# Kernel optimization log

Hardware: AMD Instinct MI355X
Metric: run time of the kernel (lower is better)

Reference implementation:

```python
import jax, jax.numpy as jnp
import numpy as np

D, K, CIN, CD, COUT = 3, 16, 128, 32, 256
C = CIN + CD                  # 160 = C_in + C_delta after concat
DM = -(-COUT // C)            # depth_multiplier = ceil(C_out / C) = 2
N, I = 4, 2048                # batch, points per cloud; M = N*I = 8192


def _bn(x, g, b, eps=1e-5):
    # BatchNorm1d in training mode: biased batch statistics over dim 0
    mu = x.mean(0)
    v = x.var(0)
    return (x - mu) * jax.lax.rsqrt(v + eps) * g + b


def _knn(p, k):
    # knn_graph over ALL M points (wrapper passes no batch vector), loop=True
    d2 = jnp.sum(p * p, axis=1)
    dist = d2[:, None] + d2[None, :] - 2.0 * (p @ p.T)   # [M,M]
    _, idx = jax.lax.top_k(-dist, k)                     # [M,K], self first
    return idx


def _gconv(t, w, b, M):
    # grouped Conv1d(K, K*K, kernel=K, groups=K): t [M,K,K], w [K(cin), K(out/grp), K(tap)]
    return jnp.einsum('mcl,col->mco', t, w).reshape(M, K * K) + b


def _xconv(xf, pf, idx, w1a, b1a, g1a, be1a, w1b, b1b, g1b, be1b,
           w2, b2, g2a, be2a, wc2a, bc2a, g2b, be2b, wc2b, bc2b, g2c, be2c,
           wcd, bcd, wl, bl):
    M = pf.shape[0]
    rel = pf[idx] - pf[:, None, :]                       # [M,K,D] relative neighbor coords
    # mlp1: lift relative coords to C_delta features
    h = rel.reshape(M * K, D)
    h = _bn(jax.nn.elu(h @ w1a + b1a), g1a, be1a)
    h = _bn(jax.nn.elu(h @ w1b + b1b), g1b, be1b)
    x_star = jnp.concatenate([h.reshape(M, K, CD), xf[idx]], axis=-1)  # [M,K,C]
    x_star = x_star.transpose(0, 2, 1)                   # [M,C,K]
    # mlp2: learn KxK X-transformation from the K*D relative coords
    t = _bn(jax.nn.elu(rel.reshape(M, K * D) @ w2 + b2), g2a, be2a).reshape(M, K, K)
    t = _bn(jax.nn.elu(_gconv(t, wc2a, bc2a, M)), g2b, be2b).reshape(M, K, K)
    t = _bn(_gconv(t, wc2b, bc2b, M), g2c, be2c).reshape(M, K, K)
    xt = jnp.einsum('mck,mkj->mcj', x_star, t)           # [M,C,K] batched matmul
    # depthwise Conv1d(C, C*DM, K, groups=C) collapses K, then final Linear
    y = jnp.einsum('mcl,col->mco', xt, wcd).reshape(M, C * DM) + bcd
    return y @ wl + bl                                   # [M,COUT]


def setup_inputs() -> dict:
    key = jax.random.key(0)
    ks = jax.random.split(key, 16)
    r = lambda k, s: jax.random.normal(k, s, jnp.float32) * 0.1
    return dict(
        x=jax.random.normal(ks[0], (N, I, CIN), jnp.float32),
        pos=jax.random.normal(ks[1], (N, I, D), jnp.float32),
        w1a=r(ks[2], (D, CD)), b1a=r(ks[3], (CD,)), g1a=jnp.ones((CD,)), be1a=jnp.zeros((CD,)),
        w1b=r(ks[4], (CD, CD)), b1b=r(ks[5], (CD,)), g1b=jnp.ones((CD,)), be1b=jnp.zeros((CD,)),
        w2=r(ks[6], (D * K, K * K)), b2=r(ks[7], (K * K,)), g2a=jnp.ones((K * K,)), be2a=jnp.zeros((K * K,)),
        wc2a=r(ks[8], (K, K, K)), bc2a=r(ks[9], (K * K,)), g2b=jnp.ones((K * K,)), be2b=jnp.zeros((K * K,)),
        wc2b=r(ks[10], (K, K, K)), bc2b=r(ks[11], (K * K,)), g2c=jnp.ones((K * K,)), be2c=jnp.zeros((K * K,)),
        wcd=r(ks[12], (C, DM, K)), bcd=r(ks[13], (C * DM,)),
        wl=r(ks[14], (C * DM, COUT)), bl=r(ks[15], (COUT,)),
    )


def reference(x, pos, w1a, b1a, g1a, be1a, w1b, b1b, g1b, be1b,
              w2, b2, g2a, be2a, wc2a, bc2a, g2b, be2b, wc2b, bc2b, g2c, be2c,
              wcd, bcd, wl, bl):
    pf = pos.reshape(N * I, D)
    xf = x.reshape(N * I, CIN)
    idx = _knn(pf, K)
    out = _xconv(xf, pf, idx, w1a, b1a, g1a, be1a, w1b, b1b, g1b, be1b,
                 w2, b2, g2a, be2a, wc2a, bc2a, g2b, be2b, wc2b, bc2b, g2c, be2c,
                 wcd, bcd, wl, bl)
    return out.reshape(N, I, COUT)
```

## Files before the change

kernel.cpp:

```cpp
#include <hip/hip_runtime.h>
#include <math.h>

#define M_PTS 8192
#define MK    131072

__device__ __forceinline__ float elu(float v){ return v > 0.f ? v : __expf(v)-1.0f; }

__device__ __forceinline__ unsigned distkey(float4 c, float qx, float qy, float qz, float d2q){
  #pragma clang fp contract(off)
  float dot  = __builtin_fmaf(c.z, qz, __builtin_fmaf(c.y, qy, __builtin_fmaf(c.x, qx, 0.0f)));
  float A    = d2q + c.w;
  float B    = 2.0f * dot;
  float dist = A - B;
  unsigned u = __float_as_uint(dist);
  return u ^ ((unsigned)((int)u >> 31) | 0x80000000u);
}

__global__ __launch_bounds__(256) void knn_kernel(const float* __restrict__ pos,
                                                  int* __restrict__ nidx,
                                                  float* __restrict__ st){
  #pragma clang fp contract(off)
  __shared__ float4 cand[1024];
  __shared__ unsigned long long hits[4][64];
  int tid  = threadIdx.x;
  int lane = tid & 63;
  int wv   = tid >> 6;
  int q    = blockIdx.x*4 + wv;
  if (blockIdx.x == 0){
    for (int i = tid; i < 2048; i += 256) st[i] = 0.f;
  }
  float qx = pos[3*q], qy = pos[3*q+1], qz = pos[3*q+2];
  float d2q = (qx*qx + qy*qy) + qz*qz;

  unsigned ka[8];
  #pragma unroll
  for (int s=0;s<8;s++) ka[s] = 0xFFFFFFFFu;

  for (int base = 0; base < M_PTS; base += 1024){
    for (int t = tid; t < 1024; t += 256){
      int j = base + t;
      float x = pos[3*j], y = pos[3*j+1], z = pos[3*j+2];
      float d2v = (x*x + y*y) + z*z;
      cand[t] = make_float4(x,y,z,d2v);
    }
    __syncthreads();
    #pragma unroll
    for (int k=0; k<16; k++){
      unsigned v = distkey(cand[lane + k*64], qx, qy, qz, d2q);
      #pragma unroll
      for (int s=0;s<8;s++){
        unsigned mn = min(v, ka[s]);
        unsigned mx = max(v, ka[s]);
        ka[s] = mn; v = mx;
      }
    }
    __syncthreads();
  }

  unsigned thr = 0xFFFFFFFFu;
  for (int r=0; r<16; r++){
    unsigned mine = ka[0];
    unsigned best = mine;
    #pragma unroll
    for (int off=32; off>0; off>>=1){
      unsigned o = __shfl_xor(best, off, 64);
      best = min(best, o);
    }
    bool adv = (best == mine);
    #pragma unroll
    for (int s=0;s<7;s++) ka[s] = adv ? ka[s+1] : ka[s];
    ka[7] = adv ? 0xFFFFFFFFu : ka[7];
    thr = best;
  }

  int cnt = 0;
  for (int base = 0; base < M_PTS; base += 1024){
    for (int t = tid; t < 1024; t += 256){
      int j = base + t;
      float x = pos[3*j], y = pos[3*j+1], z = pos[3*j+2];
      float d2v = (x*x + y*y) + z*z;
      cand[t] = make_float4(x,y,z,d2v);
    }
    __syncthreads();
    #pragma unroll
    for (int k=0; k<16; k++){
      int j = base + lane + k*64;
      unsigned u = distkey(cand[lane + k*64], qx, qy, qz, d2q);
      bool hit = (u <= thr);
      unsigned long long m = __ballot(hit);
      if (hit){
        int slot = cnt + __popcll(m & ((1ull<<lane)-1ull));
        if (slot < 64) hits[wv][slot] = ((unsigned long long)u << 32) | (unsigned)j;
      }
      cnt += (int)__popcll(m);
    }
    __syncthreads();
  }

  int cc = min(cnt, 64);
  unsigned long long mine = (lane < cc) ? hits[wv][lane] : ~0ull;
  for (int r=0; r<16; r++){
    unsigned long long best = mine;
    #pragma unroll
    for (int off=32; off>0; off>>=1){
      unsigned long long o = __shfl_xor(best, off, 64);
      best = (o < best) ? o : best;
    }
    if (mine == best) mine = ~0ull;
    if (lane == 0) nidx[q*16 + r] = (int)(unsigned)best;
  }
}

#define COMPUTE_RELF_8(OFFS)                                          \
  for (int f = tid; f < 8*48; f += 256){                              \
    int p = f/48, kd = f%48, k = kd/3, d = kd%3;                      \
    int j = nidx[(m0+p)*16 + k];                                      \
    relf[p][kd] = pos[3*j+d] - pos[3*(m0+p)+d];                       \
  }                                                                   \
  __syncthreads();

#define COMPUTE_T1_8(acc)                                             \
  _Pragma("unroll")                                                   \
  for (int p=0;p<8;p++) acc[p] = b2[tid];                             \
  for (int kk=0; kk<48; kk++){                                        \
    float w = w2[kk*256 + tid];                                       \
    _Pragma("unroll")                                                 \
    for (int p=0;p<8;p++) acc[p] += relf[p][kk]*w;                    \
  }

__global__ __launch_bounds__(256) void stats_a_kernel(const float* __restrict__ pos,
    const int* __restrict__ nidx,
    const float* __restrict__ w1a, const float* __restrict__ b1a,
    const float* __restrict__ w2,  const float* __restrict__ b2,
    float* __restrict__ s1, float* __restrict__ s3){
  int tid = threadIdx.x;
  if (blockIdx.x < 512){
    __shared__ float relS[256][3];
    __shared__ float red[8][64];
    int r = blockIdx.x*256 + tid;
    int m = r >> 4;
    int j = nidx[r];
    relS[tid][0] = pos[3*j  ]-pos[3*m  ];
    relS[tid][1] = pos[3*j+1]-pos[3*m+1];
    relS[tid][2] = pos[3*j+2]-pos[3*m+2];
    __syncthreads();
    int c = tid & 31, g = tid >> 5;
    float w0=w1a[c], w1v=w1a[32+c], w2v=w1a[64+c], b=b1a[c];
    float s=0.f, q=0.f;
    for (int rr=g*32; rr<g*32+32; rr++){
      float h = elu(b + relS[rr][0]*w0 + relS[rr][1]*w1v + relS[rr][2]*w2v);
      s += h; q += h*h;
    }
    red[g][c]=s; red[g][32+c]=q;
    __syncthreads();
    if (tid < 64){
      float a=0.f;
      #pragma unroll
      for (int gg=0;gg<8;gg++) a += red[gg][tid];
      atomicAdd(&s1[tid], a);
    }
  } else {
    __shared__ float relf[8][48];
    int m0 = (blockIdx.x-512)*8;
    COMPUTE_RELF_8();
    float acc[8];
    COMPUTE_T1_8(acc);
    float s=0.f, q=0.f;
    #pragma unroll
    for (int p=0;p<8;p++){ float v = elu(acc[p]); s += v; q += v*v; }
    atomicAdd(&s3[tid], s); atomicAdd(&s3[256+tid], q);
  }
}

__global__ __launch_bounds__(256) void stats_b_kernel(const float* __restrict__ pos,
    const int* __restrict__ nidx,
    const float* __restrict__ w1a, const float* __restrict__ b1a,
    const float* __restrict__ s1,  const float* __restrict__ g1a, const float* __restrict__ be1a,
    const float* __restrict__ w1b, const float* __restrict__ b1b,
    const float* __restrict__ w2,  const float* __restrict__ b2,
    const float* __restrict__ s3,  const float* __restrict__ g2a, const float* __restrict__ be2a,
    const float* __restrict__ wc2a,const float* __restrict__ bc2a,
    float* __restrict__ s2, float* __restrict__ s4){
  int tid = threadIdx.x;
  const float invMK = 1.f/(float)MK;
  const float invM  = 1.f/8192.f;
  if (blockIdx.x < 2048){
    __shared__ float xnS[64][33];
    __shared__ float red[8][64];
    __shared__ float muA[32], ivA[32];
    if (tid < 32){
      float mu  = s1[tid]*invMK;
      float var = s1[32+tid]*invMK - mu*mu;
      muA[tid] = mu; ivA[tid] = rsqrtf(var+1e-5f)*g1a[tid];
    }
    __syncthreads();
    {
      int rl = tid >> 2;
      int r  = blockIdx.x*64 + rl;
      int m = r >> 4;
      int j = nidx[r];
      float rx = pos[3*j]-pos[3*m], ry = pos[3*j+1]-pos[3*m+1], rz = pos[3*j+2]-pos[3*m+2];
      int c0 = (tid & 3)*8;
      #pragma unroll
      for (int u=0; u<8; u++){
        int cc = c0 + u;
        float h = elu(b1a[cc] + rx*w1a[cc] + ry*w1a[32+cc] + rz*w1a[64+cc]);
        xnS[rl][cc] = (h-muA[cc])*ivA[cc] + be1a[cc];
      }
    }
    __syncthreads();
    int o = tid & 31, g = tid >> 5;
    float wcol[32];
    #pragma unroll
    for (int cc=0;cc<32;cc++) wcol[cc] = w1b[cc*32+o];
    float bo = b1b[o], s=0.f, q=0.f;
    for (int rr=g*8; rr<g*8+8; rr++){
      float a = bo;
      #pragma unroll
      for (int cc=0;cc<32;cc++) a += xnS[rr][cc]*wcol[cc];
      float v = elu(a);
      s += v; q += v*v;
    }
    red[g][o]=s; red[g][32+o]=q;
    __syncthreads();
    if (tid < 64){
      float a=0.f;
      #pragma unroll
      for (int gg=0;gg<8;gg++) a += red[gg][tid];
      atomicAdd(&s2[tid], a);
    }
  } else {
    __shared__ float relf[8][48];
    __shared__ float tn[8][256];
    int m0 = (blockIdx.x-2048)*8;
    COMPUTE_RELF_8();
    float acc[8];
    COMPUTE_T1_8(acc);
    float mu3  = s3[tid]*invM;
    float var3 = s3[256+tid]*invM - mu3*mu3;
    float i3   = rsqrtf(var3+1e-5f)*g2a[tid];
    float bb3  = be2a[tid];
    #pragma unroll
    for (int p=0;p<8;p++) tn[p][tid] = (elu(acc[p])-mu3)*i3 + bb3;
    __syncthreads();
    int c = tid >> 4;
    float wreg[16];
    const float4* wv4 = (const float4*)(wc2a + tid*16);
    #pragma unroll
    for (int v=0; v<4; v++){ float4 f = wv4[v]; wreg[4*v]=f.x; wreg[4*v+1]=f.y; wreg[4*v+2]=f.z; wreg[4*v+3]=f.w; }
    float bias = bc2a[tid];
    float s=0.f, q=0.f;
    #pragma unroll
    for (int p=0;p<8;p++){
      float a2 = bias;
      #pragma unroll
      for (int l=0;l<16;l++) a2 += tn[p][c*16+l]*wreg[l];
      float v = elu(a2);
      s += v; q += v*v;
    }
    atomicAdd(&s4[tid], s); atomicAdd(&s4[256+tid], q);
  }
}

__global__ __launch_bounds__(256) void t3_stats_kernel(const float* __restrict__ pos,
    const int* __restrict__ nidx, const float* __restrict__ w2, const float* __restrict__ b2,
    const float* __restrict__ s3, const float* __restrict__ g2a, const float* __restrict__ be2a,
    const float* __restrict__ wc2a, const float* __restrict__ bc2a,
    const float* __restrict__ s4, const float* __restrict__ g2b, const float* __restrict__ be2b,
    const float* __restrict__ wc2b, const float* __restrict__ bc2b, float* __restrict__ s5){
  __shared__ float relf[8][48];
  __shared__ float tn[8][256];
  __shared__ float tn2[8][256];
  int m0 = blockIdx.x*8, tid = threadIdx.x;
  const float invM = 1.f/8192.f;
  COMPUTE_RELF_8();
  float acc[8];
  COMPUTE_T1_8(acc);
  float mu3  = s3[tid]*invM;
  float var3 = s3[256+tid]*invM - mu3*mu3;
  float i3   = rsqrtf(var3+1e-5f)*g2a[tid];
  float bb3  = be2a[tid];
  #pragma unroll
  for (int p=0;p<8;p++) tn[p][tid] = (elu(acc[p])-mu3)*i3 + bb3;
  __syncthreads();
  int c = tid >> 4;
  float wreg[16];
  { const float4* wv4 = (const float4*)(wc2a + tid*16);
    #pragma unroll
    for (int v=0; v<4; v++){ float4 f = wv4[v]; wreg[4*v]=f.x; wreg[4*v+1]=f.y; wreg[4*v+2]=f.z; wreg[4*v+3]=f.w; } }
  float bias = bc2a[tid];
  float mu4  = s4[tid]*invM;
  float var4 = s4[256+tid]*invM - mu4*mu4;
  float i4   = rsqrtf(var4+1e-5f)*g2b[tid];
  float bb4  = be2b[tid];
  float t2v[8];
  #pragma unroll
  for (int p=0;p<8;p++){
    float a2 = bias;
    #pragma unroll
    for (int l=0;l<16;l++) a2 += tn[p][c*16+l]*wreg[l];
    t2v[p] = elu(a2);
  }
  #pragma unroll
  for (int p=0;p<8;p++) tn2[p][tid] = (t2v[p]-mu4)*i4 + bb4;
  __syncthreads();
  float w2reg[16];
  { const float4* wv4 = (const float4*)(wc2b + tid*16);
    #pragma unroll
    for (int v=0; v<4; v++){ float4 f = wv4[v]; w2reg[4*v]=f.x; w2reg[4*v+1]=f.y; w2reg[4*v+2]=f.z; w2reg[4*v+3]=f.w; } }
  float bias2 = bc2b[tid];
  float s=0.f, q=0.f;
  #pragma unroll
  for (int p=0;p<8;p++){
    float a3 = bias2;
    #pragma unroll
    for (int l=0;l<16;l++) a3 += tn2[p][c*16+l]*w2reg[l];
    s += a3; q += a3*a3;
  }
  atomicAdd(&s5[tid], s); atomicAdd(&s5[256+tid], q);
}

#define PF 4
__global__ __launch_bounds__(256) void final_kernel(
    const float* __restrict__ x, const float* __restrict__ pos, const int* __restrict__ nidx,
    const float* __restrict__ w1a, const float* __restrict__ b1a,
    const float* __restrict__ g1a, const float* __restrict__ be1a,
    const float* __restrict__ w1b, const float* __restrict__ b1b,
    const float* __restrict__ g1b, const float* __restrict__ be1b,
    const float* __restrict__ w2,  const float* __restrict__ b2,
    const float* __restrict__ g2a, const float* __restrict__ be2a,
    const float* __restrict__ wc2a,const float* __restrict__ bc2a,
    const float* __restrict__ g2b, const float* __restrict__ be2b,
    const float* __restrict__ wc2b,const float* __restrict__ bc2b,
    const float* __restrict__ g2c, const float* __restrict__ be2c,
    const float* __restrict__ wcd, const float* __restrict__ bcd,
    const float* __restrict__ wl,  const float* __restrict__ bl,
    const float* __restrict__ st,
    float* __restrict__ out){
  __shared__ float relf[PF][48];
  __shared__ float tA[PF][256];
  __shared__ float tB[PF][256];
  __shared__ float xs[PF*32*17];
  __shared__ float yy[PF][320];
  __shared__ int   sidx[PF*16];
  __shared__ float mu1[32], i1g[32], mu2[32], i2g[32];
  int tid = threadIdx.x;
  int m0  = blockIdx.x*PF;
  const float invMK = 1.f/(float)MK;
  const float invM  = 1.f/8192.f;

  if (tid < PF*16) sidx[tid] = nidx[m0*16 + tid];
  for (int f = tid; f < PF*48; f += 256){
    int p = f/48, kd = f%48, k = kd/3, d = kd%3;
    int j = nidx[(m0+p)*16 + k];
    relf[p][kd] = pos[3*j+d] - pos[3*(m0+p)+d];
  }
  if (tid < 32){
    float mu  = st[tid]*invMK;
    float var = st[32+tid]*invMK - mu*mu;
    mu1[tid] = mu; i1g[tid] = rsqrtf(var+1e-5f)*g1a[tid];
    float mu_2  = st[64+tid]*invMK;
    float var_2 = st[96+tid]*invMK - mu_2*mu_2;
    mu2[tid] = mu_2; i2g[tid] = rsqrtf(var_2+1e-5f)*g1b[tid];
  }
  float mu3 = st[128+tid]*invM, var3 = st[384+tid]*invM - mu3*mu3;
  float i3 = rsqrtf(var3+1e-5f)*g2a[tid], bb3 = be2a[tid];
  float mu4 = st[640+tid]*invM, var4 = st[896+tid]*invM - mu4*mu4;
  float i4 = rsqrtf(var4+1e-5f)*g2b[tid], bb4 = be2b[tid];
  float mu5 = st[1152+tid]*invM, var5 = st[1408+tid]*invM - mu5*mu5;
  float i5 = rsqrtf(var5+1e-5f)*g2c[tid], bb5 = be2c[tid];
  __syncthreads();

  {
    float a[PF];
    #pragma unroll
    for (int p=0;p<PF;p++) a[p] = b2[tid];
    for (int kk=0; kk<48; kk++){
      float w = w2[kk*256 + tid];
      #pragma unroll
      for (int p=0;p<PF;p++) a[p] += relf[p][kk]*w;
    }
    #pragma unroll
    for (int p=0;p<PF;p++) tA[p][tid] = (elu(a[p])-mu3)*i3 + bb3;
  }
  __syncthreads();

  int c = tid >> 4;
  {
    float wreg[16];
    const float4* wv4 = (const float4*)(wc2a + tid*16);
    #pragma unroll
    for (int v=0; v<4; v++){ float4 f = wv4[v]; wreg[4*v]=f.x; wreg[4*v+1]=f.y; wreg[4*v+2]=f.z; wreg[4*v+3]=f.w; }
    float bias = bc2a[tid];
    float t2v[PF];
    #pragma unroll
    for (int p=0;p<PF;p++){
      float a2 = bias;
      #pragma unroll
      for (int l=0;l<16;l++) a2 += tA[p][c*16+l]*wreg[l];
      t2v[p] = elu(a2);
    }
    #pragma unroll
    for (int p=0;p<PF;p++) tB[p][tid] = (t2v[p]-mu4)*i4 + bb4;
  }
  __syncthreads();

  {
    float w2reg[16];
    const float4* wv4 = (const float4*)(wc2b + tid*16);
    #pragma unroll
    for (int v=0; v<4; v++){ float4 f = wv4[v]; w2reg[4*v]=f.x; w2reg[4*v+1]=f.y; w2reg[4*v+2]=f.z; w2reg[4*v+3]=f.w; }
    float bias2 = bc2b[tid];
    #pragma unroll
    for (int p=0;p<PF;p++){
      float a3 = bias2;
      #pragma unroll
      for (int l=0;l<16;l++) a3 += tB[p][c*16+l]*w2reg[l];
      tA[p][tid] = (a3-mu5)*i5 + bb5;
    }
  }

  {
    int row = tid >> 2;
    int p = row >> 4, k = row & 15;
    int q8 = (tid & 3)*8;
    int m = m0 + p;
    int j = sidx[p*16 + k];
    float rx = pos[3*j]-pos[3*m], ry = pos[3*j+1]-pos[3*m+1], rz = pos[3*j+2]-pos[3*m+2];
    float xn[32];
    #pragma unroll
    for (int cc=0; cc<32; cc++){
      float h = elu(b1a[cc] + rx*w1a[cc] + ry*w1a[32+cc] + rz*w1a[64+cc]);
      xn[cc] = (h-mu1[cc])*i1g[cc] + be1a[cc];
    }
    #pragma unroll
    for (int oo=0; oo<8; oo++){
      int o = q8 + oo;
      float a = b1b[o];
      #pragma unroll
      for (int cc=0; cc<32; cc++) a += xn[cc]*w1b[cc*32+o];
      float h2v = elu(a);
      xs[(p*32 + o)*17 + k] = (h2v-mu2[o])*i2g[o] + be1b[o];
    }
  }
  __syncthreads();

  for (int pair = tid; pair < PF*160; pair += 256){
    int p = pair / 160, cch = pair % 160;
    float av[16];
    if (cch < 32){
      #pragma unroll
      for (int k16=0;k16<16;k16++) av[k16] = xs[(p*32+cch)*17 + k16];
    } else {
      #pragma unroll
      for (int k16=0;k16<16;k16++) av[k16] = x[(size_t)sidx[p*16+k16]*128 + (cch-32)];
    }
    float xt[16];
    #pragma unroll
    for (int j16=0;j16<16;j16++) xt[j16]=0.f;
    #pragma unroll
    for (int k16=0;k16<16;k16++){
      float a = av[k16];
      #pragma unroll
      for (int j16=0;j16<16;j16++) xt[j16] += a*tA[p][k16*16+j16];
    }
    float y0 = bcd[cch*2], y1 = bcd[cch*2+1];
    #pragma unroll
    for (int l=0;l<16;l++){
      y0 += xt[l]*wcd[cch*32 + l];
      y1 += xt[l]*wcd[cch*32 + 16 + l];
    }
    yy[p][cch*2] = y0; yy[p][cch*2+1] = y1;
  }
  __syncthreads();

  float accO[PF];
  #pragma unroll
  for (int p=0;p<PF;p++) accO[p] = bl[tid];
  for (int q=0;q<320;q++){
    float w = wl[q*256 + tid];
    #pragma unroll
    for (int p=0;p<PF;p++) accO[p] += yy[p][q]*w;
  }
  #pragma unroll
  for (int p=0;p<PF;p++) out[(size_t)(m0+p)*256 + tid] = accO[p];
}

extern "C" void kernel_launch(void* const* d_in, const int* in_sizes, int n_in,
                              void* d_out, int out_size, void* d_ws, size_t ws_size,
                              hipStream_t stream){
  const float* x    = (const float*)d_in[0];
  const float* pos  = (const float*)d_in[1];
  const float* w1a  = (const float*)d_in[2];
  const float* b1a  = (const float*)d_in[3];
  const float* g1a  = (const float*)d_in[4];
  const float* be1a = (const float*)d_in[5];
  const float* w1b  = (const float*)d_in[6];
  const float* b1b  = (const float*)d_in[7];
  const float* g1b  = (const float*)d_in[8];
  const float* be1b = (const float*)d_in[9];
  const float* w2   = (const float*)d_in[10];
  const float* b2   = (const float*)d_in[11];
  const float* g2a  = (const float*)d_in[12];
  const float* be2a = (const float*)d_in[13];
  const float* wc2a = (const float*)d_in[14];
  const float* bc2a = (const float*)d_in[15];
  const float* g2b  = (const float*)d_in[16];
  const float* be2b = (const float*)d_in[17];
  const float* wc2b = (const float*)d_in[18];
  const float* bc2b = (const float*)d_in[19];
  const float* g2c  = (const float*)d_in[20];
  const float* be2c = (const float*)d_in[21];
  const float* wcd  = (const float*)d_in[22];
  const float* bcd  = (const float*)d_in[23];
  const float* wl   = (const float*)d_in[24];
  const float* bl   = (const float*)d_in[25];
  float* out = (float*)d_out;

  char* ws = (char*)d_ws;
  int*   nidx = (int*)(ws + 0);
  float* st   = (float*)(ws + 524288);
  float* s1 = st;
  float* s2 = st + 64;
  float* s3 = st + 128;
  float* s4 = st + 640;
  float* s5 = st + 1152;

  knn_kernel<<<2048,256,0,stream>>>(pos, nidx, st);
  stats_a_kernel<<<1536,256,0,stream>>>(pos, nidx, w1a, b1a, w2, b2, s1, s3);
  stats_b_kernel<<<3072,256,0,stream>>>(pos, nidx, w1a, b1a, s1, g1a, be1a, w1b, b1b,
                                        w2, b2, s3, g2a, be2a, wc2a, bc2a, s2, s4);
  t3_stats_kernel<<<1024,256,0,stream>>>(pos, nidx, w2, b2, s3, g2a, be2a, wc2a, bc2a,
                                         s4, g2b, be2b, wc2b, bc2b, s5);
  final_kernel<<<2048,256,0,stream>>>(x, pos, nidx,
                                      w1a, b1a, g1a, be1a, w1b, b1b, g1b, be1b,
                                      w2, b2, g2a, be2a, wc2a, bc2a,
                                      g2b, be2b, wc2b, bc2b, g2c, be2c,
                                      wcd, bcd, wl, bl, st, out);
}
```

Baseline: 404.3 us.

## Store intermediate X-transform activations in the output buffer instead of recomputing them

Each later stage used to rebuild the whole mlp2 chain from the relative coordinates: the 48x256 matmul, then the grouped convolutions. Now each stage writes its pre-norm activation into the output buffer, which serves as a scratch buffer, and the next stage reads it back and applies only the new batch-norm and one grouped conv. This removes the repeated matmul and conv work in stats_b, t3_stats and final_kernel. The cost is an extra 8 MB of global memory written and read at each stage, and correctness relies on each block of final_kernel reading its own rows of the output before it overwrites them.

```diff
diff --git a/kernel.cpp b/kernel.cpp
--- a/kernel.cpp
+++ b/kernel.cpp
@@ -111,7 +111,7 @@
   }
 }
 
-#define COMPUTE_RELF_8(OFFS)                                          \
+#define COMPUTE_RELF_8()                                              \
   for (int f = tid; f < 8*48; f += 256){                              \
     int p = f/48, kd = f%48, k = kd/3, d = kd%3;                      \
     int j = nidx[(m0+p)*16 + k];                                      \
@@ -132,6 +132,7 @@
     const int* __restrict__ nidx,
     const float* __restrict__ w1a, const float* __restrict__ b1a,
     const float* __restrict__ w2,  const float* __restrict__ b2,
+    float* __restrict__ tact,
     float* __restrict__ s1, float* __restrict__ s3){
   int tid = threadIdx.x;
   if (blockIdx.x < 512){
@@ -167,7 +168,11 @@
     COMPUTE_T1_8(acc);
     float s=0.f, q=0.f;
     #pragma unroll
-    for (int p=0;p<8;p++){ float v = elu(acc[p]); s += v; q += v*v; }
+    for (int p=0;p<8;p++){
+      float v = elu(acc[p]);
+      s += v; q += v*v;
+      tact[(size_t)(m0+p)*256 + tid] = v;
+    }
     atomicAdd(&s3[tid], s); atomicAdd(&s3[256+tid], q);
   }
 }
@@ -177,7 +182,7 @@
     const float* __restrict__ w1a, const float* __restrict__ b1a,
     const float* __restrict__ s1,  const float* __restrict__ g1a, const float* __restrict__ be1a,
     const float* __restrict__ w1b, const float* __restrict__ b1b,
-    const float* __restrict__ w2,  const float* __restrict__ b2,
+    float* __restrict__ tact,
     const float* __restrict__ s3,  const float* __restrict__ g2a, const float* __restrict__ be2a,
     const float* __restrict__ wc2a,const float* __restrict__ bc2a,
     float* __restrict__ s2, float* __restrict__ s4){
@@ -230,18 +235,17 @@
       atomicAdd(&s2[tid], a);
     }
   } else {
-    __shared__ float relf[8][48];
     __shared__ float tn[8][256];
     int m0 = (blockIdx.x-2048)*8;
-    COMPUTE_RELF_8();
-    float acc[8];
-    COMPUTE_T1_8(acc);
     float mu3  = s3[tid]*invM;
     float var3 = s3[256+tid]*invM - mu3*mu3;
     float i3   = rsqrtf(var3+1e-5f)*g2a[tid];
     float bb3  = be2a[tid];
-    #pragma unroll
-    for (int p=0;p<8;p++) tn[p][tid] = (elu(acc[p])-mu3)*i3 + bb3;
+    float tv[8];
+    #pragma unroll
+    for (int p=0;p<8;p++) tv[p] = tact[(size_t)(m0+p)*256 + tid];
+    #pragma unroll
+    for (int p=0;p<8;p++) tn[p][tid] = (tv[p]-mu3)*i3 + bb3;
     __syncthreads();
     int c = tid >> 4;
     float wreg[16];
@@ -257,53 +261,32 @@
       for (int l=0;l<16;l++) a2 += tn[p][c*16+l]*wreg[l];
       float v = elu(a2);
       s += v; q += v*v;
-    }
+      tv[p] = v;
+    }
+    #pragma unroll
+    for (int p=0;p<8;p++) tact[(size_t)(m0+p)*256 + tid] = tv[p];
     atomicAdd(&s4[tid], s); atomicAdd(&s4[256+tid], q);
   }
 }
 
-__global__ __launch_bounds__(256) void t3_stats_kernel(const float* __restrict__ pos,
-    const int* __restrict__ nidx, const float* __restrict__ w2, const float* __restrict__ b2,
-    const float* __restrict__ s3, const float* __restrict__ g2a, const float* __restrict__ be2a,
-    const float* __restrict__ wc2a, const float* __restrict__ bc2a,
+__global__ __launch_bounds__(256) void t3_stats_kernel(
+    float* __restrict__ tact,
     const float* __restrict__ s4, const float* __restrict__ g2b, const float* __restrict__ be2b,
     const float* __restrict__ wc2b, const float* __restrict__ bc2b, float* __restrict__ s5){
-  __shared__ float relf[8][48];
-  __shared__ float tn[8][256];
   __shared__ float tn2[8][256];
   int m0 = blockIdx.x*8, tid = threadIdx.x;
   const float invM = 1.f/8192.f;
-  COMPUTE_RELF_8();
-  float acc[8];
-  COMPUTE_T1_8(acc);
-  float mu3  = s3[tid]*invM;
-  float var3 = s3[256+tid]*invM - mu3*mu3;
-  float i3   = rsqrtf(var3+1e-5f)*g2a[tid];
-  float bb3  = be2a[tid];
-  #pragma unroll
-  for (int p=0;p<8;p++) tn[p][tid] = (elu(acc[p])-mu3)*i3 + bb3;
-  __syncthreads();
-  int c = tid >> 4;
-  float wreg[16];
-  { const float4* wv4 = (const float4*)(wc2a + tid*16);
-    #pragma unroll
-    for (int v=0; v<4; v++){ float4 f = wv4[v]; wreg[4*v]=f.x; wreg[4*v+1]=f.y; wreg[4*v+2]=f.z; wreg[4*v+3]=f.w; } }
-  float bias = bc2a[tid];
   float mu4  = s4[tid]*invM;
   float var4 = s4[256+tid]*invM - mu4*mu4;
   float i4   = rsqrtf(var4+1e-5f)*g2b[tid];
   float bb4  = be2b[tid];
-  float t2v[8];
-  #pragma unroll
-  for (int p=0;p<8;p++){
-    float a2 = bias;
-    #pragma unroll
-    for (int l=0;l<16;l++) a2 += tn[p][c*16+l]*wreg[l];
-    t2v[p] = elu(a2);
-  }
-  #pragma unroll
-  for (int p=0;p<8;p++) tn2[p][tid] = (t2v[p]-mu4)*i4 + bb4;
+  float tv[8];
+  #pragma unroll
+  for (int p=0;p<8;p++) tv[p] = tact[(size_t)(m0+p)*256 + tid];
+  #pragma unroll
+  for (int p=0;p<8;p++) tn2[p][tid] = (tv[p]-mu4)*i4 + bb4;
   __syncthreads();
+  int c = tid >> 4;
   float w2reg[16];
   { const float4* wv4 = (const float4*)(wc2b + tid*16);
     #pragma unroll
@@ -316,7 +299,10 @@
     #pragma unroll
     for (int l=0;l<16;l++) a3 += tn2[p][c*16+l]*w2reg[l];
     s += a3; q += a3*a3;
-  }
+    tv[p] = a3;
+  }
+  #pragma unroll
+  for (int p=0;p<8;p++) tact[(size_t)(m0+p)*256 + tid] = tv[p];
   atomicAdd(&s5[tid], s); atomicAdd(&s5[256+tid], q);
 }
 
@@ -327,19 +313,12 @@
     const float* __restrict__ g1a, const float* __restrict__ be1a,
     const float* __restrict__ w1b, const float* __restrict__ b1b,
     const float* __restrict__ g1b, const float* __restrict__ be1b,
-    const float* __restrict__ w2,  const float* __restrict__ b2,
-    const float* __restrict__ g2a, const float* __restrict__ be2a,
-    const float* __restrict__ wc2a,const float* __restrict__ bc2a,
-    const float* __restrict__ g2b, const float* __restrict__ be2b,
-    const float* __restrict__ wc2b,const float* __restrict__ bc2b,
     const float* __restrict__ g2c, const float* __restrict__ be2c,
     const float* __restrict__ wcd, const float* __restrict__ bcd,
     const float* __restrict__ wl,  const float* __restrict__ bl,
     const float* __restrict__ st,
     float* __restrict__ out){
-  __shared__ float relf[PF][48];
   __shared__ float tA[PF][256];
-  __shared__ float tB[PF][256];
   __shared__ float xs[PF*32*17];
   __shared__ float yy[PF][320];
   __shared__ int   sidx[PF*16];
@@ -350,11 +329,6 @@
   const float invM  = 1.f/8192.f;
 
   if (tid < PF*16) sidx[tid] = nidx[m0*16 + tid];
-  for (int f = tid; f < PF*48; f += 256){
-    int p = f/48, kd = f%48, k = kd/3, d = kd%3;
-    int j = nidx[(m0+p)*16 + k];
-    relf[p][kd] = pos[3*j+d] - pos[3*(m0+p)+d];
-  }
   if (tid < 32){
     float mu  = st[tid]*invMK;
     float var = st[32+tid]*invMK - mu*mu;
@@ -363,62 +337,16 @@
     float var_2 = st[96+tid]*invMK - mu_2*mu_2;
     mu2[tid] = mu_2; i2g[tid] = rsqrtf(var_2+1e-5f)*g1b[tid];
   }
-  float mu3 = st[128+tid]*invM, var3 = st[384+tid]*invM - mu3*mu3;
-  float i3 = rsqrtf(var3+1e-5f)*g2a[tid], bb3 = be2a[tid];
-  float mu4 = st[640+tid]*invM, var4 = st[896+tid]*invM - mu4*mu4;
-  float i4 = rsqrtf(var4+1e-5f)*g2b[tid], bb4 = be2b[tid];
-  float mu5 = st[1152+tid]*invM, var5 = st[1408+tid]*invM - mu5*mu5;
-  float i5 = rsqrtf(var5+1e-5f)*g2c[tid], bb5 = be2c[tid];
+  {
+    float mu5 = st[1152+tid]*invM, var5 = st[1408+tid]*invM - mu5*mu5;
+    float i5 = rsqrtf(var5+1e-5f)*g2c[tid], bb5 = be2c[tid];
+    #pragma unroll
+    for (int p=0;p<PF;p++){
+      float v = out[(size_t)(m0+p)*256 + tid];
+      tA[p][tid] = (v-mu5)*i5 + bb5;
+    }
+  }
   __syncthreads();
-
-  {
-    float a[PF];
-    #pragma unroll
-    for (int p=0;p<PF;p++) a[p] = b2[tid];
-    for (int kk=0; kk<48; kk++){
-      float w = w2[kk*256 + tid];
-      #pragma unroll
-      for (int p=0;p<PF;p++) a[p] += relf[p][kk]*w;
-    }
-    #pragma unroll
-    for (int p=0;p<PF;p++) tA[p][tid] = (elu(a[p])-mu3)*i3 + bb3;
-  }
-  __syncthreads();
-
-  int c = tid >> 4;
-  {
-    float wreg[16];
-    const float4* wv4 = (const float4*)(wc2a + tid*16);
-    #pragma unroll
-    for (int v=0; v<4; v++){ float4 f = wv4[v]; wreg[4*v]=f.x; wreg[4*v+1]=f.y; wreg[4*v+2]=f.z; wreg[4*v+3]=f.w; }
-    float bias = bc2a[tid];
-    float t2v[PF];
-    #pragma unroll
-    for (int p=0;p<PF;p++){
-      float a2 = bias;
-      #pragma unroll
-      for (int l=0;l<16;l++) a2 += tA[p][c*16+l]*wreg[l];
-      t2v[p] = elu(a2);
-    }
-    #pragma unroll
-    for (int p=0;p<PF;p++) tB[p][tid] = (t2v[p]-mu4)*i4 + bb4;
-  }
-  __syncthreads();
-
-  {
-    float w2reg[16];
-    const float4* wv4 = (const float4*)(wc2b + tid*16);
-    #pragma unroll
-    for (int v=0; v<4; v++){ float4 f = wv4[v]; w2reg[4*v]=f.x; w2reg[4*v+1]=f.y; w2reg[4*v+2]=f.z; w2reg[4*v+3]=f.w; }
-    float bias2 = bc2b[tid];
-    #pragma unroll
-    for (int p=0;p<PF;p++){
-      float a3 = bias2;
-      #pragma unroll
-      for (int l=0;l<16;l++) a3 += tB[p][c*16+l]*w2reg[l];
-      tA[p][tid] = (a3-mu5)*i5 + bb5;
-    }
-  }
 
   {
     int row = tid >> 2;
@@ -527,14 +455,11 @@
   float* s5 = st + 1152;
 
   knn_kernel<<<2048,256,0,stream>>>(pos, nidx, st);
-  stats_a_kernel<<<1536,256,0,stream>>>(pos, nidx, w1a, b1a, w2, b2, s1, s3);
+  stats_a_kernel<<<1536,256,0,stream>>>(pos, nidx, w1a, b1a, w2, b2, out, s1, s3);
   stats_b_kernel<<<3072,256,0,stream>>>(pos, nidx, w1a, b1a, s1, g1a, be1a, w1b, b1b,
-                                        w2, b2, s3, g2a, be2a, wc2a, bc2a, s2, s4);
-  t3_stats_kernel<<<1024,256,0,stream>>>(pos, nidx, w2, b2, s3, g2a, be2a, wc2a, bc2a,
-                                         s4, g2b, be2b, wc2b, bc2b, s5);
+                                        out, s3, g2a, be2a, wc2a, bc2a, s2, s4);
+  t3_stats_kernel<<<1024,256,0,stream>>>(out, s4, g2b, be2b, wc2b, bc2b, s5);
   final_kernel<<<2048,256,0,stream>>>(x, pos, nidx,
                                       w1a, b1a, g1a, be1a, w1b, b1b, g1b, be1b,
-                                      w2, b2, g2a, be2a, wc2a, bc2a,
-                                      g2b, be2b, wc2b, bc2b, g2c, be2c,
-                                      wcd, bcd, wl, bl, st, out);
-}
+                                      g2c, be2c, wcd, bcd, wl, bl, st, out);
+}
```

Result: faster. 389.4 us (-3.7%).
